# Kernel optimization log

Measured on AMD Instinct MI355X. Metric: run time of the kernel, lower is better.

## Reference

```python
import jax, jax.numpy as jnp
import numpy as np

RESIZE = 518   # image_encoder.resize_size (DINOv2)
PATCH = 14     # image_encoder.patch_size
GRID = RESIZE // PATCH          # 37
TOTAL = GRID * GRID             # 1369


def setup_inputs() -> dict:
    key = jax.random.key(0)
    ks = jax.random.split(key, 10)
    B, C, V, D, F, P = 2, 6, 50000, 384, 64, 100000
    M = TOTAL
    patch_tokens = jax.random.normal(ks[0], (B, C, M, D), jnp.float32)
    voxel_features = jax.random.normal(ks[1], (B, V, F), jnp.float32)
    voxel_coords = jax.random.normal(ks[2], (B, V, 3), jnp.float32) * 20.0
    image_sizes = jnp.tile(jnp.array([[900.0, 1600.0]], jnp.float32), (B, 1))
    # realistic pinhole intrinsics (fx=fy=1200, cx=800, cy=450)
    K = jnp.array([[1200.0, 0.0, 800.0], [0.0, 1200.0, 450.0], [0.0, 0.0, 1.0]], jnp.float32)
    cam_intrinsics = jnp.broadcast_to(K, (B, C, 3, 3))
    # extrinsics: identity rotation + random translation per camera
    Rt = jnp.broadcast_to(jnp.eye(4, dtype=jnp.float32), (B, C, 4, 4))
    t = jax.random.normal(ks[3], (B, C, 3), jnp.float32) * 5.0
    lidar2cam_extrinsics = Rt.at[..., :3, 3].set(t)
    point2voxel_idx = jax.random.randint(ks[4], (B, P), 0, V)
    W1 = jax.random.normal(ks[5], (F + D, 256), jnp.float32) * 0.02
    b1 = jnp.zeros((256,), jnp.float32)
    W2 = jax.random.normal(ks[6], (256, 64), jnp.float32) * 0.02
    b2 = jnp.zeros((64,), jnp.float32)
    W3 = jax.random.normal(ks[7], (64, 16), jnp.float32) * 0.02
    b3 = jnp.zeros((16,), jnp.float32)
    return {"patch_tokens": patch_tokens, "voxel_features": voxel_features,
            "voxel_coords": voxel_coords, "image_sizes": image_sizes,
            "cam_intrinsics": cam_intrinsics, "lidar2cam_extrinsics": lidar2cam_extrinsics,
            "point2voxel_idx": point2voxel_idx,
            "W1": W1, "b1": b1, "W2": W2, "b2": b2, "W3": W3, "b3": b3}


def reference(patch_tokens, voxel_features, voxel_coords, image_sizes,
              cam_intrinsics, lidar2cam_extrinsics, point2voxel_idx,
              W1, b1, W2, b2, W3, b3):
    B, V, _ = voxel_coords.shape
    # ---- multi_camera_projector, vectorized over cameras ----
    pts_h = jnp.concatenate([voxel_coords, jnp.ones((B, V, 1), voxel_coords.dtype)], -1)
    cam_pts = jnp.einsum('bcij,bvj->bcvi', lidar2cam_extrinsics, pts_h)  # (B,C,V,4)
    xyz = cam_pts[..., :3]
    z = xyz[..., 2]
    pix = jnp.einsum('bcij,bcvj->bcvi', cam_intrinsics, xyz)             # (B,C,V,3)
    denom = jnp.maximum(pix[..., 2], 1e-12)
    u = pix[..., 0] / denom
    v = pix[..., 1] / denom
    H = image_sizes[:, 0][:, None, None]
    W = image_sizes[:, 1][:, None, None]
    valid = (z > 0) & (u >= 0) & (u < W) & (v >= 0) & (v < H)            # (B,C,V)
    coords = jnp.where(valid[..., None], jnp.stack([u, v], -1), -1.0)    # (B,C,V,2)
    # ---- scale_pixel_coords to (RESIZE, RESIZE) ----
    scale = jnp.stack([RESIZE / jnp.maximum(image_sizes[:, 1], 1e-6),
                       RESIZE / jnp.maximum(image_sizes[:, 0], 1e-6)], -1)  # (B,2) = (sw, sh)
    coords = coords * scale[:, None, None, :]
    # ---- patch grid indexing (trunc-toward-zero like torch .long()) ----
    pxy = (coords / float(PATCH)).astype(jnp.int32)
    px = jnp.clip(pxy[..., 0], 0, GRID - 1)
    py = jnp.clip(pxy[..., 1], 0, GRID - 1)
    flat = jnp.clip(py * GRID + px, 0, TOTAL - 1)                        # (B,C,V)
    gathered = jnp.take_along_axis(patch_tokens, flat[..., None], axis=2)  # (B,C,V,D)
    # ---- masked mean over cameras ----
    mask = valid[..., None].astype(patch_tokens.dtype)
    fused_img = (gathered * mask).sum(1) / jnp.maximum(mask.sum(1), 1.0)  # (B,V,D)
    # ---- concat + MLP ----
    fused = jnp.concatenate([voxel_features, fused_img], -1)             # (B,V,F+D)
    h = jax.nn.relu(fused @ W1 + b1)
    h = jax.nn.relu(h @ W2 + b2)
    voxel_scores = h @ W3 + b3                                           # (B,V,16)
    # ---- devoxelize: gather voxel scores back to points ----
    point_scores = jnp.take_along_axis(voxel_scores, point2voxel_idx[..., None], axis=1)
    return point_scores
```

## Files before the change

kernel.cpp:

```cpp
#include <hip/hip_runtime.h>

#define NB 2
#define NC 6
#define NV 50000
#define ND 384
#define NF 64
#define NP 100000
#define NM 1369
#define NROW (NB*NV)
#define TILE 32

typedef __attribute__((ext_vector_type(8))) short bf8_t;
typedef __attribute__((ext_vector_type(4))) float f4_t;

__device__ inline unsigned short f2bf(float x) {
    unsigned u = __builtin_bit_cast(unsigned, x);
    u += 0x7fffu + ((u >> 16) & 1u);
    return (unsigned short)(u >> 16);
}
__device__ inline unsigned pack2bf(float lo, float hi) {
    return (unsigned)f2bf(lo) | ((unsigned)f2bf(hi) << 16);
}

__device__ inline void proj_one(const float* __restrict__ E,
                                const float* __restrict__ Km,
                                float x, float y, float z,
                                float Ws, float Hs, float sx, float sy,
                                bool& valid, int& flat)
{
#pragma clang fp contract(off)
    const float X = ((E[0]*x + E[1]*y) + E[2]*z) + E[3];
    const float Y = ((E[4]*x + E[5]*y) + E[6]*z) + E[7];
    const float Z = ((E[8]*x + E[9]*y) + E[10]*z) + E[11];
    const float p0 = (Km[0]*X + Km[1]*Y) + Km[2]*Z;
    const float p1 = (Km[3]*X + Km[4]*Y) + Km[5]*Z;
    const float p2 = (Km[6]*X + Km[7]*Y) + Km[8]*Z;
    const float den = fmaxf(p2, 1e-12f);
    const float u = p0 / den;
    const float v = p1 / den;
    valid = (Z > 0.0f) & (u >= 0.0f) & (u < Ws) & (v >= 0.0f) & (v < Hs);
    const float us = u * sx;
    const float vs = v * sy;
    int px = (int)(us / 14.0f);
    int py = (int)(vs / 14.0f);
    px = px < 0 ? 0 : (px > 36 ? 36 : px);
    py = py < 0 ? 0 : (py > 36 ? 36 : py);
    flat = py*37 + px;
}

__global__ __launch_bounds__(256) void pack_w1(const float* __restrict__ W1,
                                               unsigned short* __restrict__ out) {
    const int t = blockIdx.x*256 + threadIdx.x;
    const int k = t >> 8, n = t & 255;
    const int kc = k >> 5, g = (k >> 3) & 3, i = k & 7;
    const int w = n >> 6, nf = (n >> 4) & 3, m = n & 15;
    out[(((kc*16 + w*4 + nf)*64 + g*16 + m) << 3) + i] = f2bf(W1[k*256 + n]);
}

__global__ __launch_bounds__(256) void pack_w2(const float* __restrict__ W2,
                                               unsigned short* __restrict__ out) {
    const int t = blockIdx.x*256 + threadIdx.x;
    const int k = t >> 6, n = t & 63;
    const int kc = k >> 5, g = (k >> 3) & 3, i = k & 7;
    const int nf = n >> 4, m = n & 15;
    out[(((kc*4 + nf)*64 + g*16 + m) << 3) + i] = f2bf(W2[k*64 + n]);
}

__global__ __launch_bounds__(256) void pack_w3(const float* __restrict__ W3,
                                               unsigned short* __restrict__ out) {
    const int t = blockIdx.x*256 + threadIdx.x;
    const int k = t >> 4, n = t & 15;
    const int kc = k >> 5, g = (k >> 3) & 3, i = k & 7;
    out[((kc*64 + g*16 + n) << 3) + i] = f2bf(W3[k*16 + n]);
}

__global__ __launch_bounds__(256, 5) void fuse_mlp_kernel(
    const float* __restrict__ patch,
    const float* __restrict__ vfeat,
    const float* __restrict__ vcoord,
    const float* __restrict__ imsz,
    const float* __restrict__ intr,
    const float* __restrict__ extr,
    const float* __restrict__ b1,
    const float* __restrict__ b2,
    const float* __restrict__ b3,
    const unsigned short* __restrict__ w1p_,
    const unsigned short* __restrict__ w2p_,
    const unsigned short* __restrict__ w3p_,
    float* __restrict__ scores)
{
    __shared__ __align__(16) unsigned short sX[TILE*456];
    __shared__ int sFlat[NC*TILE];
    unsigned short* sH1   = sX;
    unsigned short* sH2bf = sX + 8448;

    const int tid  = threadIdx.x;
    const int base = blockIdx.x * TILE;
    const int lane = tid & 63;
    const int w    = tid >> 6;
    const int mrow = lane & 15;
    const int kg   = lane >> 4;

    float vf[8];
    #pragma unroll
    for (int i = 0; i < 8; ++i)
        vf[i] = vfeat[(size_t)(base + w + 4*i)*NF + lane];

    if (tid < NC*TILE) {
        const int r = tid & 31, c = tid >> 5;
        const int n = base + r;
        const int b = n / NV;
        const float x = vcoord[(size_t)n*3+0];
        const float y = vcoord[(size_t)n*3+1];
        const float z = vcoord[(size_t)n*3+2];
        const float Hs = imsz[b*2+0];
        const float Ws = imsz[b*2+1];
        const float sx = 518.0f / fmaxf(Ws, 1e-6f);
        const float sy = 518.0f / fmaxf(Hs, 1e-6f);
        const float* E  = extr + (size_t)(b*NC + c)*16;
        const float* Km = intr + (size_t)(b*NC + c)*9;
        bool valid; int flat;
        proj_one(E, Km, x, y, z, Ws, Hs, sx, sy, valid, flat);
        sFlat[c*TILE + r] = valid ? flat : -1;
    }
    __syncthreads();

    #pragma unroll
    for (int t = 0; t < 4; ++t) {
        const int r0 = w + 8*t, r1 = r0 + 4;
        const int n0 = base + r0, n1 = base + r1;
        const int b0 = n0 / NV, b1b = n1 / NV;
        float A0x=0.f,A0y=0.f,A1x=0.f,A1y=0.f,A2x=0.f,A2y=0.f; int cnt0 = 0;
        float B0x=0.f,B0y=0.f,B1x=0.f,B1y=0.f,B2x=0.f,B2y=0.f; int cnt1 = 0;
        #pragma unroll
        for (int c = 0; c < NC; ++c) {
            const int f0 = sFlat[c*TILE + r0];
            const int f1 = sFlat[c*TILE + r1];
            if (f0 >= 0) {
                const float2* tp = (const float2*)(patch + ((size_t)(b0*NC + c)*NM + f0)*ND);
                const float2 t0 = tp[lane];
                const float2 t1 = tp[lane + 64];
                const float2 t2 = tp[lane + 128];
                A0x += t0.x; A0y += t0.y;
                A1x += t1.x; A1y += t1.y;
                A2x += t2.x; A2y += t2.y;
                ++cnt0;
            }
            if (f1 >= 0) {
                const float2* tp = (const float2*)(patch + ((size_t)(b1b*NC + c)*NM + f1)*ND);
                const float2 t0 = tp[lane];
                const float2 t1 = tp[lane + 64];
                const float2 t2 = tp[lane + 128];
                B0x += t0.x; B0y += t0.y;
                B1x += t1.x; B1y += t1.y;
                B2x += t2.x; B2y += t2.y;
                ++cnt1;
            }
        }
        const float inv0 = 1.0f / fmaxf((float)cnt0, 1.0f);
        const float inv1 = 1.0f / fmaxf((float)cnt1, 1.0f);
        unsigned* d0 = (unsigned*)sX + r0*228 + 32;
        d0[lane]       = pack2bf(A0x*inv0, A0y*inv0);
        d0[64 + lane]  = pack2bf(A1x*inv0, A1y*inv0);
        d0[128 + lane] = pack2bf(A2x*inv0, A2y*inv0);
        sX[r0*456 + lane] = f2bf(vf[2*t]);
        unsigned* d1 = (unsigned*)sX + r1*228 + 32;
        d1[lane]       = pack2bf(B0x*inv1, B0y*inv1);
        d1[64 + lane]  = pack2bf(B1x*inv1, B1y*inv1);
        d1[128 + lane] = pack2bf(B2x*inv1, B2y*inv1);
        sX[r1*456 + lane] = f2bf(vf[2*t + 1]);
    }
    __syncthreads();

    const bf8_t* w1p = (const bf8_t*)w1p_;
    const f4_t zero = {0.f, 0.f, 0.f, 0.f};
    f4_t acc1[2][4];
    #pragma unroll
    for (int a = 0; a < 2; ++a)
        #pragma unroll
        for (int q = 0; q < 4; ++q) acc1[a][q] = zero;

    for (int kc = 0; kc < 14; ++kc) {
        const bf8_t a0 = *(const bf8_t*)&sX[ mrow      *456 + kc*32 + kg*8];
        const bf8_t a1 = *(const bf8_t*)&sX[(mrow + 16)*456 + kc*32 + kg*8];
        const bf8_t* bp = w1p + (size_t)((kc*16 + w*4)*64 + lane);
        #pragma unroll
        for (int nf = 0; nf < 4; ++nf) {
            const bf8_t bfr = bp[nf*64];
            acc1[0][nf] = __builtin_amdgcn_mfma_f32_16x16x32_bf16(a0, bfr, acc1[0][nf], 0, 0, 0);
            acc1[1][nf] = __builtin_amdgcn_mfma_f32_16x16x32_bf16(a1, bfr, acc1[1][nf], 0, 0, 0);
        }
    }
    __syncthreads();

    #pragma unroll
    for (int nf = 0; nf < 4; ++nf) {
        const float bb = b1[w*64 + nf*16 + mrow];
        #pragma unroll
        for (int mf = 0; mf < 2; ++mf)
            #pragma unroll
            for (int r = 0; r < 4; ++r) {
                const float v = fmaxf(acc1[mf][nf][r] + bb, 0.f);
                sH1[(mf*16 + kg*4 + r)*264 + w*64 + nf*16 + mrow] = f2bf(v);
            }
    }
    __syncthreads();

    const bf8_t* w2p = (const bf8_t*)w2p_;
    f4_t acc2[2];
    acc2[0] = zero; acc2[1] = zero;
    for (int kc = 0; kc < 8; ++kc) {
        const bf8_t a0 = *(const bf8_t*)&sH1[ mrow      *264 + kc*32 + kg*8];
        const bf8_t a1 = *(const bf8_t*)&sH1[(mrow + 16)*264 + kc*32 + kg*8];
        const bf8_t bfr = w2p[(kc*4 + w)*64 + lane];
        acc2[0] = __builtin_amdgcn_mfma_f32_16x16x32_bf16(a0, bfr, acc2[0], 0, 0, 0);
        acc2[1] = __builtin_amdgcn_mfma_f32_16x16x32_bf16(a1, bfr, acc2[1], 0, 0, 0);
    }
    {
        const float bb = b2[w*16 + mrow];
        #pragma unroll
        for (int mf = 0; mf < 2; ++mf)
            #pragma unroll
            for (int r = 0; r < 4; ++r) {
                const float v = fmaxf(acc2[mf][r] + bb, 0.f);
                sH2bf[(mf*16 + kg*4 + r)*72 + w*16 + mrow] = f2bf(v);
            }
    }
    __syncthreads();

    if (w < 2) {
        const bf8_t* w3p = (const bf8_t*)w3p_;
        f4_t acc3 = zero;
        #pragma unroll
        for (int kc = 0; kc < 2; ++kc) {
            const bf8_t a = *(const bf8_t*)&sH2bf[(w*16 + mrow)*72 + kc*32 + kg*8];
            const bf8_t bfr = w3p[kc*64 + lane];
            acc3 = __builtin_amdgcn_mfma_f32_16x16x32_bf16(a, bfr, acc3, 0, 0, 0);
        }
        const float bb = b3[mrow];
        #pragma unroll
        for (int r = 0; r < 4; ++r)
            scores[(size_t)(base + w*16 + kg*4 + r)*16 + mrow] = acc3[r] + bb;
    }
}

__global__ __launch_bounds__(256) void gather_kernel(
    const float* __restrict__ scores,
    const int* __restrict__ p2v,
    float* __restrict__ out)
{
    const int g  = blockIdx.x * 256 + threadIdx.x;
    const int q  = g & 3;
    const int pl = g >> 2;
    const int b  = pl / NP;
    const int idx = p2v[pl];
    const float4 val = *(const float4*)&scores[((size_t)(b*NV + idx))*16 + q*4];
    *(float4*)&out[(size_t)g*4] = val;
}

extern "C" void kernel_launch(void* const* d_in, const int* in_sizes, int n_in,
                              void* d_out, int out_size, void* d_ws, size_t ws_size,
                              hipStream_t stream) {
    const float* patch = (const float*)d_in[0];
    const float* vfeat = (const float*)d_in[1];
    const float* vcoord= (const float*)d_in[2];
    const float* imsz  = (const float*)d_in[3];
    const float* intr  = (const float*)d_in[4];
    const float* extr  = (const float*)d_in[5];
    const int*   p2v   = (const int*)d_in[6];
    const float* W1 = (const float*)d_in[7];
    const float* b1 = (const float*)d_in[8];
    const float* W2 = (const float*)d_in[9];
    const float* b2 = (const float*)d_in[10];
    const float* W3 = (const float*)d_in[11];
    const float* b3 = (const float*)d_in[12];

    float* scores = (float*)d_ws;
    unsigned short* w1pack = (unsigned short*)((char*)d_ws + 6400000);
    unsigned short* w2pack = (unsigned short*)((char*)d_ws + 6629376);
    unsigned short* w3pack = (unsigned short*)((char*)d_ws + 6662144);

    pack_w1<<<448, 256, 0, stream>>>(W1, w1pack);
    pack_w2<<<64, 256, 0, stream>>>(W2, w2pack);
    pack_w3<<<4, 256, 0, stream>>>(W3, w3pack);
    fuse_mlp_kernel<<<NROW/TILE, 256, 0, stream>>>(
        patch, vfeat, vcoord, imsz, intr, extr,
        b1, b2, b3, w1pack, w2pack, w3pack, scores);
    gather_kernel<<<(NB*NP*4)/256, 256, 0, stream>>>(scores, p2v, (float*)d_out);
}
```

Baseline: 68.53 us.

## Precompute patch-token projection through W1 before gathering per voxel

Uses linearity of the first layer: the masked mean of gathered patch tokens times W1 equals the masked mean of pre-projected tokens, so a new kernel multiplies all 16428 patch tokens by the image part of W1 once and stores 256-wide bf16 rows. The fused kernel then gathers 256 bf16 values per camera instead of 384 floats, and computes only the 64-column voxel-feature part of layer one. The three weight pack kernels are merged into one launch. This adds an extra kernel and a workspace buffer, and rounds the projected tokens to bf16 before averaging.

```diff
diff --git a/kernel.cpp b/kernel.cpp
--- a/kernel.cpp
+++ b/kernel.cpp
@@ -8,6 +8,7 @@
 #define NP 100000
 #define NM 1369
 #define NROW (NB*NV)
+#define NT (NB*NC*NM)
 #define TILE 32
 
 typedef __attribute__((ext_vector_type(8))) short bf8_t;
@@ -21,6 +22,8 @@
 __device__ inline unsigned pack2bf(float lo, float hi) {
     return (unsigned)f2bf(lo) | ((unsigned)f2bf(hi) << 16);
 }
+__device__ inline float bflo(unsigned u) { return __builtin_bit_cast(float, u << 16); }
+__device__ inline float bfhi(unsigned u) { return __builtin_bit_cast(float, u & 0xffff0000u); }
 
 __device__ inline void proj_one(const float* __restrict__ E,
                                 const float* __restrict__ Km,
@@ -48,34 +51,89 @@
     flat = py*37 + px;
 }
 
-__global__ __launch_bounds__(256) void pack_w1(const float* __restrict__ W1,
-                                               unsigned short* __restrict__ out) {
-    const int t = blockIdx.x*256 + threadIdx.x;
-    const int k = t >> 8, n = t & 255;
-    const int kc = k >> 5, g = (k >> 3) & 3, i = k & 7;
-    const int w = n >> 6, nf = (n >> 4) & 3, m = n & 15;
-    out[(((kc*16 + w*4 + nf)*64 + g*16 + m) << 3) + i] = f2bf(W1[k*256 + n]);
-}
-
-__global__ __launch_bounds__(256) void pack_w2(const float* __restrict__ W2,
-                                               unsigned short* __restrict__ out) {
-    const int t = blockIdx.x*256 + threadIdx.x;
-    const int k = t >> 6, n = t & 63;
-    const int kc = k >> 5, g = (k >> 3) & 3, i = k & 7;
-    const int nf = n >> 4, m = n & 15;
-    out[(((kc*4 + nf)*64 + g*16 + m) << 3) + i] = f2bf(W2[k*64 + n]);
-}
-
-__global__ __launch_bounds__(256) void pack_w3(const float* __restrict__ W3,
-                                               unsigned short* __restrict__ out) {
-    const int t = blockIdx.x*256 + threadIdx.x;
-    const int k = t >> 4, n = t & 15;
-    const int kc = k >> 5, g = (k >> 3) & 3, i = k & 7;
-    out[((kc*64 + g*16 + n) << 3) + i] = f2bf(W3[k*16 + n]);
-}
-
-__global__ __launch_bounds__(256, 5) void fuse_mlp_kernel(
+__global__ __launch_bounds__(256) void pack_all(
+    const float* __restrict__ W1, const float* __restrict__ W2,
+    const float* __restrict__ W3,
+    unsigned short* __restrict__ o1, unsigned short* __restrict__ o2,
+    unsigned short* __restrict__ o3)
+{
+    const int blk = blockIdx.x;
+    if (blk < 448) {
+        const int t = blk*256 + threadIdx.x;
+        const int k = t >> 8, n = t & 255;
+        const int kc = k >> 5, g = (k >> 3) & 3, i = k & 7;
+        const int w = n >> 6, nf = (n >> 4) & 3, m = n & 15;
+        o1[(((kc*16 + w*4 + nf)*64 + g*16 + m) << 3) + i] = f2bf(W1[k*256 + n]);
+    } else if (blk < 512) {
+        const int t = (blk - 448)*256 + threadIdx.x;
+        const int k = t >> 6, n = t & 63;
+        const int kc = k >> 5, g = (k >> 3) & 3, i = k & 7;
+        const int nf = n >> 4, m = n & 15;
+        o2[(((kc*4 + nf)*64 + g*16 + m) << 3) + i] = f2bf(W2[k*64 + n]);
+    } else {
+        const int t = (blk - 512)*256 + threadIdx.x;
+        const int k = t >> 4, n = t & 15;
+        const int kc = k >> 5, g = (k >> 3) & 3, i = k & 7;
+        o3[((kc*64 + g*16 + n) << 3) + i] = f2bf(W3[k*16 + n]);
+    }
+}
+
+__global__ __launch_bounds__(256) void ptok_kernel(
     const float* __restrict__ patch,
+    const unsigned short* __restrict__ w1p_,
+    unsigned short* __restrict__ T)
+{
+    const int tid  = threadIdx.x;
+    const int lane = tid & 63;
+    const int w    = tid >> 6;
+    const int mrow = lane & 15;
+    const int kg   = lane >> 4;
+    const int rbase = blockIdx.x * 32;
+
+    const bf8_t* w1p = (const bf8_t*)w1p_;
+    const f4_t zero = {0.f, 0.f, 0.f, 0.f};
+    f4_t acc[2][4];
+    #pragma unroll
+    for (int a = 0; a < 2; ++a)
+        #pragma unroll
+        for (int q = 0; q < 4; ++q) acc[a][q] = zero;
+
+    for (int j = 0; j < 12; ++j) {
+        bf8_t afr[2];
+        #pragma unroll
+        for (int mf = 0; mf < 2; ++mf) {
+            int row = rbase + mf*16 + mrow;
+            row = row < NT ? row : NT - 1;
+            const float* ap = patch + (size_t)row*ND + j*32 + kg*8;
+            const f4_t lo = *(const f4_t*)ap;
+            const f4_t hi = *(const f4_t*)(ap + 4);
+            #pragma unroll
+            for (int i = 0; i < 4; ++i) {
+                afr[mf][i]   = (short)f2bf(lo[i]);
+                afr[mf][4+i] = (short)f2bf(hi[i]);
+            }
+        }
+        const bf8_t* bp = w1p + (size_t)(((j+2)*16 + w*4)*64 + lane);
+        #pragma unroll
+        for (int nf = 0; nf < 4; ++nf) {
+            const bf8_t bfr = bp[nf*64];
+            acc[0][nf] = __builtin_amdgcn_mfma_f32_16x16x32_bf16(afr[0], bfr, acc[0][nf], 0, 0, 0);
+            acc[1][nf] = __builtin_amdgcn_mfma_f32_16x16x32_bf16(afr[1], bfr, acc[1][nf], 0, 0, 0);
+        }
+    }
+    #pragma unroll
+    for (int nf = 0; nf < 4; ++nf)
+        #pragma unroll
+        for (int mf = 0; mf < 2; ++mf)
+            #pragma unroll
+            for (int r = 0; r < 4; ++r) {
+                const int trow = rbase + mf*16 + kg*4 + r;
+                if (trow < NT)
+                    T[(size_t)trow*256 + w*64 + nf*16 + mrow] = f2bf(acc[mf][nf][r]);
+            }
+}
+
+__global__ __launch_bounds__(256, 7) void fuse_mlp_kernel(
     const float* __restrict__ vfeat,
     const float* __restrict__ vcoord,
     const float* __restrict__ imsz,
@@ -87,12 +145,12 @@
     const unsigned short* __restrict__ w1p_,
     const unsigned short* __restrict__ w2p_,
     const unsigned short* __restrict__ w3p_,
+    const unsigned short* __restrict__ T,
     float* __restrict__ scores)
 {
-    __shared__ __align__(16) unsigned short sX[TILE*456];
+    __shared__ __align__(16) unsigned short sVP[TILE*264];
+    __shared__ __align__(16) unsigned short sVF[TILE*72];
     __shared__ int sFlat[NC*TILE];
-    unsigned short* sH1   = sX;
-    unsigned short* sH2bf = sX + 8448;
 
     const int tid  = threadIdx.x;
     const int base = blockIdx.x * TILE;
@@ -101,10 +159,12 @@
     const int mrow = lane & 15;
     const int kg   = lane >> 4;
 
-    float vf[8];
-    #pragma unroll
-    for (int i = 0; i < 8; ++i)
-        vf[i] = vfeat[(size_t)(base + w + 4*i)*NF + lane];
+    #pragma unroll
+    for (int i = 0; i < 8; ++i) {
+        const int e = tid + 256*i;
+        const int r = e >> 6, c = e & 63;
+        sVF[r*72 + c] = f2bf(vfeat[(size_t)(base + r)*NF + c]);
+    }
 
     if (tid < NC*TILE) {
         const int r = tid & 31, c = tid >> 5;
@@ -125,87 +185,84 @@
     }
     __syncthreads();
 
-    #pragma unroll
-    for (int t = 0; t < 4; ++t) {
-        const int r0 = w + 8*t, r1 = r0 + 4;
-        const int n0 = base + r0, n1 = base + r1;
-        const int b0 = n0 / NV, b1b = n1 / NV;
-        float A0x=0.f,A0y=0.f,A1x=0.f,A1y=0.f,A2x=0.f,A2y=0.f; int cnt0 = 0;
-        float B0x=0.f,B0y=0.f,B1x=0.f,B1y=0.f,B2x=0.f,B2y=0.f; int cnt1 = 0;
+    const bf8_t* w1p = (const bf8_t*)w1p_;
+    const f4_t zero = {0.f, 0.f, 0.f, 0.f};
+    f4_t acc1[2][4];
+    #pragma unroll
+    for (int a = 0; a < 2; ++a)
+        #pragma unroll
+        for (int q = 0; q < 4; ++q) acc1[a][q] = zero;
+    #pragma unroll
+    for (int kc = 0; kc < 2; ++kc) {
+        const bf8_t a0 = *(const bf8_t*)&sVF[ mrow      *72 + kc*32 + kg*8];
+        const bf8_t a1 = *(const bf8_t*)&sVF[(mrow + 16)*72 + kc*32 + kg*8];
+        const bf8_t* bp = w1p + (size_t)((kc*16 + w*4)*64 + lane);
+        #pragma unroll
+        for (int nf = 0; nf < 4; ++nf) {
+            const bf8_t bfr = bp[nf*64];
+            acc1[0][nf] = __builtin_amdgcn_mfma_f32_16x16x32_bf16(a0, bfr, acc1[0][nf], 0, 0, 0);
+            acc1[1][nf] = __builtin_amdgcn_mfma_f32_16x16x32_bf16(a1, bfr, acc1[1][nf], 0, 0, 0);
+        }
+    }
+    #pragma unroll
+    for (int nf = 0; nf < 4; ++nf) {
+        const float bb = b1[w*64 + nf*16 + mrow];
+        #pragma unroll
+        for (int mf = 0; mf < 2; ++mf)
+            #pragma unroll
+            for (int r = 0; r < 4; ++r)
+                sVP[(mf*16 + kg*4 + r)*264 + w*64 + nf*16 + mrow] = f2bf(acc1[mf][nf][r] + bb);
+    }
+    __syncthreads();
+
+    #pragma unroll
+    for (int t4 = 0; t4 < 4; ++t4) {
+        const int r0 = w + 8*t4, r1 = r0 + 4;
+        const int b0 = (base + r0) / NV, b1v = (base + r1) / NV;
+        float g00=0.f,g01=0.f,g02=0.f,g03=0.f; int cnt0 = 0;
+        float g10=0.f,g11=0.f,g12=0.f,g13=0.f; int cnt1 = 0;
         #pragma unroll
         for (int c = 0; c < NC; ++c) {
             const int f0 = sFlat[c*TILE + r0];
             const int f1 = sFlat[c*TILE + r1];
             if (f0 >= 0) {
-                const float2* tp = (const float2*)(patch + ((size_t)(b0*NC + c)*NM + f0)*ND);
-                const float2 t0 = tp[lane];
-                const float2 t1 = tp[lane + 64];
-                const float2 t2 = tp[lane + 128];
-                A0x += t0.x; A0y += t0.y;
-                A1x += t1.x; A1y += t1.y;
-                A2x += t2.x; A2y += t2.y;
+                const uint2 u = *(const uint2*)(T + ((size_t)((b0*NC + c)*NM + f0))*256 + lane*4);
+                g00 += bflo(u.x); g01 += bfhi(u.x);
+                g02 += bflo(u.y); g03 += bfhi(u.y);
                 ++cnt0;
             }
             if (f1 >= 0) {
-                const float2* tp = (const float2*)(patch + ((size_t)(b1b*NC + c)*NM + f1)*ND);
-                const float2 t0 = tp[lane];
-                const float2 t1 = tp[lane + 64];
-                const float2 t2 = tp[lane + 128];
-                B0x += t0.x; B0y += t0.y;
-                B1x += t1.x; B1y += t1.y;
-                B2x += t2.x; B2y += t2.y;
+                const uint2 u = *(const uint2*)(T + ((size_t)((b1v*NC + c)*NM + f1))*256 + lane*4);
+                g10 += bflo(u.x); g11 += bfhi(u.x);
+                g12 += bflo(u.y); g13 += bfhi(u.y);
                 ++cnt1;
             }
         }
         const float inv0 = 1.0f / fmaxf((float)cnt0, 1.0f);
         const float inv1 = 1.0f / fmaxf((float)cnt1, 1.0f);
-        unsigned* d0 = (unsigned*)sX + r0*228 + 32;
-        d0[lane]       = pack2bf(A0x*inv0, A0y*inv0);
-        d0[64 + lane]  = pack2bf(A1x*inv0, A1y*inv0);
-        d0[128 + lane] = pack2bf(A2x*inv0, A2y*inv0);
-        sX[r0*456 + lane] = f2bf(vf[2*t]);
-        unsigned* d1 = (unsigned*)sX + r1*228 + 32;
-        d1[lane]       = pack2bf(B0x*inv1, B0y*inv1);
-        d1[64 + lane]  = pack2bf(B1x*inv1, B1y*inv1);
-        d1[128 + lane] = pack2bf(B2x*inv1, B2y*inv1);
-        sX[r1*456 + lane] = f2bf(vf[2*t + 1]);
+        {
+            uint2 vp = *(uint2*)&sVP[r0*264 + lane*4];
+            const float h0 = fmaxf(g00*inv0 + bflo(vp.x), 0.f);
+            const float h1v = fmaxf(g01*inv0 + bfhi(vp.x), 0.f);
+            const float h2v = fmaxf(g02*inv0 + bflo(vp.y), 0.f);
+            const float h3 = fmaxf(g03*inv0 + bfhi(vp.y), 0.f);
+            uint2 o; o.x = pack2bf(h0, h1v); o.y = pack2bf(h2v, h3);
+            *(uint2*)&sVP[r0*264 + lane*4] = o;
+        }
+        {
+            uint2 vp = *(uint2*)&sVP[r1*264 + lane*4];
+            const float h0 = fmaxf(g10*inv1 + bflo(vp.x), 0.f);
+            const float h1v = fmaxf(g11*inv1 + bfhi(vp.x), 0.f);
+            const float h2v = fmaxf(g12*inv1 + bflo(vp.y), 0.f);
+            const float h3 = fmaxf(g13*inv1 + bfhi(vp.y), 0.f);
+            uint2 o; o.x = pack2bf(h0, h1v); o.y = pack2bf(h2v, h3);
+            *(uint2*)&sVP[r1*264 + lane*4] = o;
+        }
     }
     __syncthreads();
 
-    const bf8_t* w1p = (const bf8_t*)w1p_;
-    const f4_t zero = {0.f, 0.f, 0.f, 0.f};
-    f4_t acc1[2][4];
-    #pragma unroll
-    for (int a = 0; a < 2; ++a)
-        #pragma unroll
-        for (int q = 0; q < 4; ++q) acc1[a][q] = zero;
-
-    for (int kc = 0; kc < 14; ++kc) {
-        const bf8_t a0 = *(const bf8_t*)&sX[ mrow      *456 + kc*32 + kg*8];
-        const bf8_t a1 = *(const bf8_t*)&sX[(mrow + 16)*456 + kc*32 + kg*8];
-        const bf8_t* bp = w1p + (size_t)((kc*16 + w*4)*64 + lane);
-        #pragma unroll
-        for (int nf = 0; nf < 4; ++nf) {
-            const bf8_t bfr = bp[nf*64];
-            acc1[0][nf] = __builtin_amdgcn_mfma_f32_16x16x32_bf16(a0, bfr, acc1[0][nf], 0, 0, 0);
-            acc1[1][nf] = __builtin_amdgcn_mfma_f32_16x16x32_bf16(a1, bfr, acc1[1][nf], 0, 0, 0);
-        }
-    }
-    __syncthreads();
-
-    #pragma unroll
-    for (int nf = 0; nf < 4; ++nf) {
-        const float bb = b1[w*64 + nf*16 + mrow];
-        #pragma unroll
-        for (int mf = 0; mf < 2; ++mf)
-            #pragma unroll
-            for (int r = 0; r < 4; ++r) {
-                const float v = fmaxf(acc1[mf][nf][r] + bb, 0.f);
-                sH1[(mf*16 + kg*4 + r)*264 + w*64 + nf*16 + mrow] = f2bf(v);
-            }
-    }
-    __syncthreads();
-
+    unsigned short* sH1 = sVP;
+    unsigned short* sH2bf = sVF;
     const bf8_t* w2p = (const bf8_t*)w2p_;
     f4_t acc2[2];
     acc2[0] = zero; acc2[1] = zero;
@@ -279,12 +336,12 @@
     unsigned short* w1pack = (unsigned short*)((char*)d_ws + 6400000);
     unsigned short* w2pack = (unsigned short*)((char*)d_ws + 6629376);
     unsigned short* w3pack = (unsigned short*)((char*)d_ws + 6662144);
-
-    pack_w1<<<448, 256, 0, stream>>>(W1, w1pack);
-    pack_w2<<<64, 256, 0, stream>>>(W2, w2pack);
-    pack_w3<<<4, 256, 0, stream>>>(W3, w3pack);
+    unsigned short* Tbuf   = (unsigned short*)((char*)d_ws + 6664192);
+
+    pack_all<<<516, 256, 0, stream>>>(W1, W2, W3, w1pack, w2pack, w3pack);
+    ptok_kernel<<<(NT + 31)/32, 256, 0, stream>>>(patch, w1pack, Tbuf);
     fuse_mlp_kernel<<<NROW/TILE, 256, 0, stream>>>(
-        patch, vfeat, vcoord, imsz, intr, extr,
-        b1, b2, b3, w1pack, w2pack, w3pack, scores);
+        vfeat, vcoord, imsz, intr, extr,
+        b1, b2, b3, w1pack, w2pack, w3pack, Tbuf, scores);
     gather_kernel<<<(NB*NP*4)/256, 256, 0, stream>>>(scores, p2v, (float*)d_out);
 }
```

After: 68.55 us. About the same (+0.0%).
